# Kernel tuning notes

Measured on AMD Instinct MI355X. Metric: run time of the kernel, lower is better.

## Reference

```python
import jax, jax.numpy as jnp
import numpy as np

DIM = 768
HEADS = 12
SCALE = DIM ** (-0.5)  # NOTE: original scales by full dim, not per-head dim


def setup_inputs() -> dict:
    key = jax.random.key(0)
    k1, k2, k3 = jax.random.split(key, 3)
    b, n = 4, 2048
    x = jax.random.normal(k1, (b, n, DIM), dtype=jnp.float32)
    # torch Linear layout: weight [out_features, in_features]
    w_qkv = jax.random.normal(k2, (3 * DIM, DIM), dtype=jnp.float32) * (DIM ** -0.5)
    b_qkv = jnp.zeros((3 * DIM,), dtype=jnp.float32)
    w_out = jax.random.normal(k3, (DIM, DIM), dtype=jnp.float32) * (DIM ** -0.5)
    b_out = jnp.zeros((DIM,), dtype=jnp.float32)
    return {"x": x, "w_qkv": w_qkv, "b_qkv": b_qkv, "w_out": w_out, "b_out": b_out}


def reference(x, w_qkv, b_qkv, w_out, b_out):
    b, n, dim = x.shape
    h = HEADS
    d = dim // h
    qkv = x @ w_qkv.T + b_qkv                       # [b, n, 3*dim]
    # rearrange 'b n (qkv h d) -> qkv b h n d'
    qkv = qkv.reshape(b, n, 3, h, d).transpose(2, 0, 3, 1, 4)
    q, k, v = qkv[0], qkv[1], qkv[2]                # each [b, h, n, d]
    dots = jnp.einsum('bhid,bhjd->bhij', q, k) * SCALE
    attn = jax.nn.softmax(dots, axis=-1)
    out = jnp.einsum('bhij,bhjd->bhid', attn, v)    # [b, h, n, d]
    out = out.transpose(0, 2, 1, 3).reshape(b, n, h * d)
    out = out @ w_out.T + b_out
    return out
```

## Files before the change

### kernel.cpp

```cpp
#include <hip/hip_runtime.h>
#include <hip/hip_bf16.h>
#include <stdint.h>
#include <math.h>

#define HEADS 12
#define HD 64
#define NB 4
#define NSEQ 2048
#define DIM 768
#define MROWS (NB*NSEQ)
#define QKV_OUT (3*DIM)
#define SCALE 0.03608439182435161f
#define QSCALE (0.03608439182435161f * 1.4426950408889634f)
#define RESCALE_THR 8.0f

typedef __bf16 bf16;
typedef __attribute__((ext_vector_type(8))) __bf16 bf16x8;
typedef __attribute__((ext_vector_type(4))) __bf16 bf16x4;
typedef __attribute__((ext_vector_type(4))) float f32x4;
typedef __attribute__((ext_vector_type(16))) float f32x16;
typedef unsigned int uint;

typedef __attribute__((address_space(1))) void gvoid_t;
typedef __attribute__((address_space(3))) void lvoid_t;
#define GLOAD_LDS16(src, dst) \
  __builtin_amdgcn_global_load_lds((gvoid_t*)(src), (lvoid_t*)(dst), 16, 0, 0)

__device__ __forceinline__ float max3f(float a, float b, float c) {
  return fmaxf(fmaxf(a, b), c);
}
__device__ __forceinline__ float fast_exp2(float x) {
  float r; asm("v_exp_f32 %0, %1" : "=v"(r) : "v"(x)); return r;
}

__global__ void k_cvt3(const float* __restrict__ x, const float* __restrict__ wqkv,
                       const float* __restrict__ wout,
                       bf16* __restrict__ xb, bf16* __restrict__ wqkvb,
                       bf16* __restrict__ woutb) {
  const int n0 = MROWS * DIM / 4, n1 = QKV_OUT * DIM / 4, n2 = DIM * DIM / 4;
  int i = blockIdx.x * blockDim.x + threadIdx.x;
  const float* src; bf16* dst;
  if (i < n0)           { src = x;    dst = xb; }
  else if (i < n0 + n1) { src = wqkv; dst = wqkvb; i -= n0; }
  else if (i < n0 + n1 + n2) { src = wout; dst = woutb; i -= n0 + n1; }
  else return;
  const f32x4 v = ((const f32x4*)src)[i];
  bf16x4 o;
#pragma unroll
  for (int j = 0; j < 4; ++j) o[j] = (bf16)v[j];
  ((bf16x4*)dst)[i] = o;
}

template<int ROWBYTES>
__device__ __forceinline__ void stage_swz(const bf16* g, int grow0, int gstride,
                                          int gcol0, char* ldsbuf) {
  constexpr int CPR = ROWBYTES / 16;
  const int t = threadIdx.x;
  const int wid = t >> 6;
#pragma unroll
  for (int call = 0; call < 2; ++call) {
    const int o = call * 4096 + t * 16;
    const int r = o / ROWBYTES;
    const int c = (o % ROWBYTES) / 16;
    const int cs = c ^ (r & (CPR - 1));
    const bf16* src = g + (long)(grow0 + r) * gstride + gcol0 + cs * 8;
    char* dst = ldsbuf + call * 4096 + wid * 1024;
    GLOAD_LDS16(src, dst);
  }
}

template<int ROWBYTES>
__device__ __forceinline__ bf16x8 frag_ld(const char* buf, int row, int chunk) {
  constexpr int CPR = ROWBYTES / 16;
  const int cs = chunk ^ (row & (CPR - 1));
  return *(const bf16x8*)(buf + row * ROWBYTES + cs * 16);
}

__device__ __forceinline__ uint cvtpk_bf16(float a, float b) {
  uint r; asm("v_cvt_pk_bf16_f32 %0, %1, %2" : "=v"(r) : "v"(a), "v"(b)); return r;
}
__device__ __forceinline__ void plswap(uint &a, uint &b) {
  asm("v_permlane32_swap_b32 %0, %1" : "+v"(a), "+v"(b));
}
__device__ __forceinline__ void build_pfrags(const f32x16 &p, bf16x8 *f) {
  union { uint u[4]; bf16x8 v; } A, B;
  uint a0 = cvtpk_bf16(p[0], p[1]),  b0 = cvtpk_bf16(p[4], p[5]);   plswap(a0, b0);
  uint a1 = cvtpk_bf16(p[2], p[3]),  b1 = cvtpk_bf16(p[6], p[7]);   plswap(a1, b1);
  A.u[0] = a0; A.u[1] = a1; A.u[2] = b0; A.u[3] = b1;
  uint a2 = cvtpk_bf16(p[8], p[9]),  b2 = cvtpk_bf16(p[12], p[13]); plswap(a2, b2);
  uint a3 = cvtpk_bf16(p[10], p[11]), b3 = cvtpk_bf16(p[14], p[15]); plswap(a3, b3);
  B.u[0] = a2; B.u[1] = a3; B.u[2] = b2; B.u[3] = b3;
  f[0] = A.v; f[1] = B.v;
}

__device__ __forceinline__ void gemm_core(const bf16* __restrict__ A, const bf16* __restrict__ Bm,
                                          int m0, int n0, f32x4 acc[4][4], char* lds) {
  const int t = threadIdx.x;
  const int lane = t & 63, wid = t >> 6;
  const int lr = lane & 15, l4 = lane >> 4;
  const int wm = wid >> 1, wn = wid & 1;
#pragma unroll
  for (int i = 0; i < 4; ++i)
#pragma unroll
    for (int j = 0; j < 4; ++j) acc[i][j] = f32x4{0.f, 0.f, 0.f, 0.f};

  stage_swz<64>(A, m0, DIM, 0, lds);
  stage_swz<64>(Bm, n0, DIM, 0, lds + 16384);
  __syncthreads();
  int cur = 0;
  const int NT = DIM / 32;
  for (int kt = 0; kt < NT; ++kt) {
    char* Acur = lds + cur * 8192;
    char* Bcur = lds + 16384 + cur * 8192;
    if (kt + 1 < NT) {
      stage_swz<64>(A, m0, DIM, (kt + 1) * 32, lds + (cur ^ 1) * 8192);
      stage_swz<64>(Bm, n0, DIM, (kt + 1) * 32, lds + 16384 + (cur ^ 1) * 8192);
    }
    bf16x8 af[4], bfr[4];
#pragma unroll
    for (int i = 0; i < 4; ++i) af[i] = frag_ld<64>(Acur, wm * 64 + i * 16 + lr, l4);
#pragma unroll
    for (int j = 0; j < 4; ++j) bfr[j] = frag_ld<64>(Bcur, wn * 64 + j * 16 + lr, l4);
#pragma unroll
    for (int i = 0; i < 4; ++i)
#pragma unroll
      for (int j = 0; j < 4; ++j)
        acc[i][j] = __builtin_amdgcn_mfma_f32_16x16x32_bf16(af[i], bfr[j], acc[i][j], 0, 0, 0);
    __syncthreads();
    cur ^= 1;
  }
}

__global__ void __launch_bounds__(256) k_qkv_gemm(const bf16* __restrict__ xb,
                                                  const bf16* __restrict__ wb,
                                                  const float* __restrict__ bqkv,
                                                  bf16* __restrict__ qb,
                                                  bf16* __restrict__ kb,
                                                  bf16* __restrict__ vtb) {
  __shared__ alignas(128) char lds[32768];
  const int m0 = blockIdx.x * 128;
  const int n0 = blockIdx.y * 128;
  f32x4 acc[4][4];
  gemm_core(xb, wb, m0, n0, acc, lds);

  const int t = threadIdx.x;
  const int lane = t & 63, wid = t >> 6;
  const int lr = lane & 15, l4 = lane >> 4;
  const int wm = wid >> 1, wn = wid & 1;
#pragma unroll
  for (int j = 0; j < 4; ++j) {
    const int o = n0 + wn * 64 + j * 16 + lr;
    const float bias = bqkv[o];
    const int region = o / DIM;
    const int oc = o - region * DIM;
    const int h = oc >> 6, d = oc & 63;
#pragma unroll
    for (int i = 0; i < 4; ++i) {
      const int mb = m0 + wm * 64 + i * 16 + l4 * 4;
      const int bb = mb >> 11;
      const int nn = mb & 2047;
      if (region == 2) {
        bf16x4 pk;
#pragma unroll
        for (int r = 0; r < 4; ++r) pk[r] = (bf16)(acc[i][j][r] + bias);
        *(bf16x4*)(vtb + ((long)((bb * HEADS + h) * HD + d)) * NSEQ + nn) = pk;
      } else {
#pragma unroll
        for (int r = 0; r < 4; ++r) {
          const float v = acc[i][j][r] + bias;
          const long idx = ((long)((bb * HEADS + h) * NSEQ + (nn + r))) * HD + d;
          if (region == 0) qb[idx] = (bf16)(v * QSCALE);
          else             kb[idx] = (bf16)v;
        }
      }
    }
  }
}

__global__ void __launch_bounds__(256) k_attn(const bf16* __restrict__ qb,
                                              const bf16* __restrict__ kb,
                                              const bf16* __restrict__ vtb,
                                              bf16* __restrict__ ob) {
  __shared__ alignas(128) char lds[32768];
  const int bh = blockIdx.x;
  const int qt = blockIdx.y;
  const int t = threadIdx.x;
  const int lane = t & 63, wid = t >> 6;
  const int l31 = lane & 31, hi = lane >> 5;
  const bf16* qg = qb + (long)bh * NSEQ * HD;
  const bf16* kg = kb + (long)bh * NSEQ * HD;
  const bf16* vg = vtb + (long)bh * HD * NSEQ;
  const int q0w = qt * 128 + wid * 32;

  bf16x8 bq[4];
#pragma unroll
  for (int ks = 0; ks < 4; ++ks)
    bq[ks] = *(const bf16x8*)(qg + (long)(q0w + l31) * HD + ks * 16 + hi * 8);

  f32x16 ot0, ot1;
#pragma unroll
  for (int r = 0; r < 16; ++r) { ot0[r] = 0.f; ot1[r] = 0.f; }
  float m_run = -1.0e30f, l_run = 0.f;

  stage_swz<128>(kg, 0, HD, 0, lds);
  stage_swz<128>(vg, 0, NSEQ, 0, lds + 16384);
  __syncthreads();
  int cur = 0;
  for (int kt = 0; kt < NSEQ / 64; ++kt) {
    char* Kcur = lds + cur * 8192;
    char* Vcur = lds + 16384 + cur * 8192;
    if (kt + 1 < NSEQ / 64) {
      stage_swz<128>(kg, (kt + 1) * 64, HD, 0, lds + (cur ^ 1) * 8192);
      stage_swz<128>(vg, 0, NSEQ, (kt + 1) * 64, lds + 16384 + (cur ^ 1) * 8192);
    }
    f32x16 s0, s1;
#pragma unroll
    for (int r = 0; r < 16; ++r) { s0[r] = 0.f; s1[r] = 0.f; }
    __builtin_amdgcn_s_setprio(1);
#pragma unroll
    for (int ks = 0; ks < 4; ++ks) {
      const bf16x8 ak0 = frag_ld<128>(Kcur, l31, ks * 2 + hi);
      s0 = __builtin_amdgcn_mfma_f32_32x32x16_bf16(ak0, bq[ks], s0, 0, 0, 0);
      const bf16x8 ak1 = frag_ld<128>(Kcur, 32 + l31, ks * 2 + hi);
      s1 = __builtin_amdgcn_mfma_f32_32x32x16_bf16(ak1, bq[ks], s1, 0, 0, 0);
    }
    __builtin_amdgcn_s_setprio(0);
    float u0 = max3f(s0[0], s0[1], s0[2]);
    float u1 = max3f(s0[3], s0[4], s0[5]);
    float u2 = max3f(s0[6], s0[7], s0[8]);
    float u3 = max3f(s0[9], s0[10], s0[11]);
    float u4 = max3f(s0[12], s0[13], s0[14]);
    float u5 = max3f(s0[15], s1[0], s1[1]);
    float u6 = max3f(s1[2], s1[3], s1[4]);
    float u7 = max3f(s1[5], s1[6], s1[7]);
    float u8 = max3f(s1[8], s1[9], s1[10]);
    float u9 = max3f(s1[11], s1[12], s1[13]);
    float ua = fmaxf(s1[14], s1[15]);
    u0 = max3f(u0, u1, u2);
    u3 = max3f(u3, u4, u5);
    u6 = max3f(u6, u7, u8);
    u9 = max3f(u9, ua, u0);
    float mx = max3f(u3, u6, u9);
    mx = fmaxf(mx, __shfl_xor(mx, 32));
    if (__any(mx - m_run > RESCALE_THR)) {
      const float mn = fmaxf(m_run, mx);
      const float alpha = fast_exp2(m_run - mn);
      m_run = mn;
      l_run *= alpha;
#pragma unroll
      for (int r = 0; r < 16; ++r) { ot0[r] *= alpha; ot1[r] *= alpha; }
    }
    float rs0 = 0.f, rs1 = 0.f;
#pragma unroll
    for (int r = 0; r < 16; ++r) {
      s0[r] = fast_exp2(s0[r] - m_run); rs0 += s0[r];
      s1[r] = fast_exp2(s1[r] - m_run); rs1 += s1[r];
    }
    float rs = rs0 + rs1;
    rs += __shfl_xor(rs, 32);
    l_run += rs;
    bf16x8 pf[4];
    build_pfrags(s0, &pf[0]);
    build_pfrags(s1, &pf[2]);
    __builtin_amdgcn_s_setprio(1);
#pragma unroll
    for (int s = 0; s < 4; ++s) {
      const bf16x8 av0 = frag_ld<128>(Vcur, l31, s * 2 + hi);
      ot0 = __builtin_amdgcn_mfma_f32_32x32x16_bf16(av0, pf[s], ot0, 0, 0, 0);
      const bf16x8 av1 = frag_ld<128>(Vcur, 32 + l31, s * 2 + hi);
      ot1 = __builtin_amdgcn_mfma_f32_32x32x16_bf16(av1, pf[s], ot1, 0, 0, 0);
    }
    __builtin_amdgcn_s_setprio(0);
    __syncthreads();
    cur ^= 1;
  }
  const float inv = 1.f / l_run;
#pragma unroll
  for (int r = 0; r < 16; ++r) { ot0[r] *= inv; ot1[r] *= inv; }
  __syncthreads();
  char* tw = lds + wid * 4352;
#pragma unroll
  for (int g = 0; g < 4; ++g) {
    uint2 w0, w1;
    w0.x = cvtpk_bf16(ot0[4 * g], ot0[4 * g + 1]);
    w0.y = cvtpk_bf16(ot0[4 * g + 2], ot0[4 * g + 3]);
    w1.x = cvtpk_bf16(ot1[4 * g], ot1[4 * g + 1]);
    w1.y = cvtpk_bf16(ot1[4 * g + 2], ot1[4 * g + 3]);
    const int d0 = 8 * g + 4 * hi;
    *(uint2*)(tw + l31 * 136 + d0 * 2) = w0;
    *(uint2*)(tw + l31 * 136 + (32 + d0) * 2) = w1;
  }
  const int b_ = bh / HEADS, h_ = bh - b_ * HEADS;
#pragma unroll
  for (int pass = 0; pass < 4; ++pass) {
    const int row = pass * 8 + (lane >> 3);
    const bf16x8 vv = *(const bf16x8*)(tw + row * 136 + (lane & 7) * 16);
    *(bf16x8*)(ob + ((long)(b_ * NSEQ + q0w + row)) * DIM + h_ * 64 + (lane & 7) * 8) = vv;
  }
}

__global__ void __launch_bounds__(256) k_out_gemm(const bf16* __restrict__ ab,
                                                  const bf16* __restrict__ wob,
                                                  const float* __restrict__ bout,
                                                  float* __restrict__ out) {
  __shared__ alignas(128) char lds[32768];
  const int m0 = blockIdx.x * 128;
  const int n0 = blockIdx.y * 128;
  f32x4 acc[4][4];
  gemm_core(ab, wob, m0, n0, acc, lds);

  const int t = threadIdx.x;
  const int lane = t & 63, wid = t >> 6;
  const int lr = lane & 15, l4 = lane >> 4;
  const int wm = wid >> 1, wn = wid & 1;
#pragma unroll
  for (int j = 0; j < 4; ++j) {
    const int o = n0 + wn * 64 + j * 16 + lr;
    const float bias = bout[o];
#pragma unroll
    for (int i = 0; i < 4; ++i) {
      const int mb = m0 + wm * 64 + i * 16 + l4 * 4;
#pragma unroll
      for (int r = 0; r < 4; ++r)
        out[(long)(mb + r) * DIM + o] = acc[i][j][r] + bias;
    }
  }
}

extern "C" void kernel_launch(void* const* d_in, const int* in_sizes, int n_in,
                              void* d_out, int out_size, void* d_ws, size_t ws_size,
                              hipStream_t stream) {
  const float* x    = (const float*)d_in[0];
  const float* wqkv = (const float*)d_in[1];
  const float* bqkv = (const float*)d_in[2];
  const float* wout = (const float*)d_in[3];
  const float* bout = (const float*)d_in[4];
  float* out = (float*)d_out;
  char* ws = (char*)d_ws;

  bf16* xb    = (bf16*)(ws);
  bf16* wqkvb = (bf16*)(ws + 12582912);
  bf16* woutb = (bf16*)(ws + 16121856);
  bf16* qb    = (bf16*)(ws + 17301504);
  bf16* kb    = (bf16*)(ws + 29884416);
  bf16* vtb   = (bf16*)(ws + 42467328);
  bf16* ab    = (bf16*)(ws + 55050240);

  const int ncvt4 = MROWS * DIM / 4 + QKV_OUT * DIM / 4 + DIM * DIM / 4;
  k_cvt3<<<(ncvt4 + 255) / 256, 256, 0, stream>>>(x, wqkv, wout, xb, wqkvb, woutb);

  k_qkv_gemm<<<dim3(MROWS / 128, QKV_OUT / 128), 256, 0, stream>>>(xb, wqkvb, bqkv, qb, kb, vtb);
  k_attn<<<dim3(NB * HEADS, NSEQ / 128), 256, 0, stream>>>(qb, kb, vtb, ab);
  k_out_gemm<<<dim3(MROWS / 128, DIM / 128), 256, 0, stream>>>(ab, woutb, bout, out);
}
```

Measured before the change: 156.1 us.

## Swap GEMM operand order for vectorized epilogue stores and hoist attention staging addresses

```diff
diff --git a/kernel.cpp b/kernel.cpp
--- a/kernel.cpp
+++ b/kernel.cpp
@@ -10,7 +10,6 @@
 #define DIM 768
 #define MROWS (NB*NSEQ)
 #define QKV_OUT (3*DIM)
-#define SCALE 0.03608439182435161f
 #define QSCALE (0.03608439182435161f * 1.4426950408889634f)
 #define RESCALE_THR 8.0f
 
@@ -31,6 +30,12 @@
 }
 __device__ __forceinline__ float fast_exp2(float x) {
   float r; asm("v_exp_f32 %0, %1" : "=v"(r) : "v"(x)); return r;
+}
+__device__ __forceinline__ uint cvtpk_bf16(float a, float b) {
+  uint r; asm("v_cvt_pk_bf16_f32 %0, %1, %2" : "=v"(r) : "v"(a), "v"(b)); return r;
+}
+__device__ __forceinline__ void plswap(uint &a, uint &b) {
+  asm("v_permlane32_swap_b32 %0, %1" : "+v"(a), "+v"(b));
 }
 
 __global__ void k_cvt3(const float* __restrict__ x, const float* __restrict__ wqkv,
@@ -76,12 +81,6 @@
   return *(const bf16x8*)(buf + row * ROWBYTES + cs * 16);
 }
 
-__device__ __forceinline__ uint cvtpk_bf16(float a, float b) {
-  uint r; asm("v_cvt_pk_bf16_f32 %0, %1, %2" : "=v"(r) : "v"(a), "v"(b)); return r;
-}
-__device__ __forceinline__ void plswap(uint &a, uint &b) {
-  asm("v_permlane32_swap_b32 %0, %1" : "+v"(a), "+v"(b));
-}
 __device__ __forceinline__ void build_pfrags(const f32x16 &p, bf16x8 *f) {
   union { uint u[4]; bf16x8 v; } A, B;
   uint a0 = cvtpk_bf16(p[0], p[1]),  b0 = cvtpk_bf16(p[4], p[5]);   plswap(a0, b0);
@@ -140,38 +139,52 @@
   __shared__ alignas(128) char lds[32768];
   const int m0 = blockIdx.x * 128;
   const int n0 = blockIdx.y * 128;
-  f32x4 acc[4][4];
-  gemm_core(xb, wb, m0, n0, acc, lds);
-
+  const int region = n0 / DIM;
   const int t = threadIdx.x;
   const int lane = t & 63, wid = t >> 6;
   const int lr = lane & 15, l4 = lane >> 4;
   const int wm = wid >> 1, wn = wid & 1;
-#pragma unroll
-  for (int j = 0; j < 4; ++j) {
-    const int o = n0 + wn * 64 + j * 16 + lr;
-    const float bias = bqkv[o];
-    const int region = o / DIM;
-    const int oc = o - region * DIM;
-    const int h = oc >> 6, d = oc & 63;
-#pragma unroll
-    for (int i = 0; i < 4; ++i) {
-      const int mb = m0 + wm * 64 + i * 16 + l4 * 4;
-      const int bb = mb >> 11;
-      const int nn = mb & 2047;
-      if (region == 2) {
+  f32x4 acc[4][4];
+
+  if (region < 2) {
+    gemm_core(wb, xb, n0, m0, acc, lds);
+    bf16* dst0 = (region == 0) ? qb : kb;
+#pragma unroll
+    for (int j = 0; j < 4; ++j) {
+      const int mb = m0 + wn * 64 + j * 16 + lr;
+      const int bb = mb >> 11, nn = mb & 2047;
+#pragma unroll
+      for (int i = 0; i < 4; ++i) {
+        const int o = n0 + wm * 64 + i * 16 + l4 * 4;
+        const f32x4 b4 = *(const f32x4*)(bqkv + o);
+        const int oc = o - region * DIM;
+        const int h = oc >> 6, d = oc & 63;
+        bf16x4 pk;
+#pragma unroll
+        for (int r = 0; r < 4; ++r) {
+          float v = acc[i][j][r] + b4[r];
+          if (region == 0) v *= QSCALE;
+          pk[r] = (bf16)v;
+        }
+        *(bf16x4*)(dst0 + ((long)((bb * HEADS + h) * NSEQ + nn)) * HD + d) = pk;
+      }
+    }
+  } else {
+    gemm_core(xb, wb, m0, n0, acc, lds);
+#pragma unroll
+    for (int j = 0; j < 4; ++j) {
+      const int o = n0 + wn * 64 + j * 16 + lr;
+      const float bias = bqkv[o];
+      const int oc = o - 2 * DIM;
+      const int h = oc >> 6, d = oc & 63;
+#pragma unroll
+      for (int i = 0; i < 4; ++i) {
+        const int mb = m0 + wm * 64 + i * 16 + l4 * 4;
+        const int bb = mb >> 11, nn = mb & 2047;
         bf16x4 pk;
 #pragma unroll
         for (int r = 0; r < 4; ++r) pk[r] = (bf16)(acc[i][j][r] + bias);
         *(bf16x4*)(vtb + ((long)((bb * HEADS + h) * HD + d)) * NSEQ + nn) = pk;
-      } else {
-#pragma unroll
-        for (int r = 0; r < 4; ++r) {
-          const float v = acc[i][j][r] + bias;
-          const long idx = ((long)((bb * HEADS + h) * NSEQ + (nn + r))) * HD + d;
-          if (region == 0) qb[idx] = (bf16)(v * QSCALE);
-          else             kb[idx] = (bf16)v;
-        }
       }
     }
   }
@@ -182,6 +195,7 @@
                                               const bf16* __restrict__ vtb,
                                               bf16* __restrict__ ob) {
   __shared__ alignas(128) char lds[32768];
+  char* ldsc = lds;
   const int bh = blockIdx.x;
   const int qt = blockIdx.y;
   const int t = threadIdx.x;
@@ -197,31 +211,49 @@
   for (int ks = 0; ks < 4; ++ks)
     bq[ks] = *(const bf16x8*)(qg + (long)(q0w + l31) * HD + ks * 16 + hi * 8);
 
+  const int rbase = l31 * 128 + (((hi ^ l31) & 7) << 4);
+
+  const int o0 = t * 16, o1 = 4096 + t * 16;
+  const int r0 = o0 >> 7, cs0 = ((o0 & 127) >> 4) ^ (r0 & 7);
+  const int r1 = o1 >> 7, cs1 = ((o1 & 127) >> 4) ^ (r1 & 7);
+  const bf16* ksA = kg + r0 * 64 + cs0 * 8;
+  const bf16* ksB = kg + r1 * 64 + cs1 * 8;
+  const bf16* vsA = vg + (long)r0 * NSEQ + cs0 * 8;
+  const bf16* vsB = vg + (long)r1 * NSEQ + cs1 * 8;
+  const int dofs = wid << 10;
+
   f32x16 ot0, ot1;
 #pragma unroll
   for (int r = 0; r < 16; ++r) { ot0[r] = 0.f; ot1[r] = 0.f; }
   float m_run = -1.0e30f, l_run = 0.f;
 
-  stage_swz<128>(kg, 0, HD, 0, lds);
-  stage_swz<128>(vg, 0, NSEQ, 0, lds + 16384);
+  GLOAD_LDS16(ksA, ldsc + dofs);
+  GLOAD_LDS16(ksB, ldsc + 4096 + dofs);
+  GLOAD_LDS16(vsA, ldsc + 16384 + dofs);
+  GLOAD_LDS16(vsB, ldsc + 20480 + dofs);
   __syncthreads();
   int cur = 0;
   for (int kt = 0; kt < NSEQ / 64; ++kt) {
-    char* Kcur = lds + cur * 8192;
-    char* Vcur = lds + 16384 + cur * 8192;
     if (kt + 1 < NSEQ / 64) {
-      stage_swz<128>(kg, (kt + 1) * 64, HD, 0, lds + (cur ^ 1) * 8192);
-      stage_swz<128>(vg, 0, NSEQ, (kt + 1) * 64, lds + 16384 + (cur ^ 1) * 8192);
-    }
+      const int nb = (cur ^ 1) << 13;
+      const int ko = (kt + 1) * 4096;
+      const int vo = (kt + 1) * 64;
+      GLOAD_LDS16(ksA + ko, ldsc + nb + dofs);
+      GLOAD_LDS16(ksB + ko, ldsc + nb + 4096 + dofs);
+      GLOAD_LDS16(vsA + vo, ldsc + nb + 16384 + dofs);
+      GLOAD_LDS16(vsB + vo, ldsc + nb + 20480 + dofs);
+    }
+    const int tb = rbase + (cur << 13);
     f32x16 s0, s1;
 #pragma unroll
     for (int r = 0; r < 16; ++r) { s0[r] = 0.f; s1[r] = 0.f; }
     __builtin_amdgcn_s_setprio(1);
 #pragma unroll
     for (int ks = 0; ks < 4; ++ks) {
-      const bf16x8 ak0 = frag_ld<128>(Kcur, l31, ks * 2 + hi);
+      const int a = tb ^ (ks << 5);
+      const bf16x8 ak0 = *(const bf16x8*)(ldsc + a);
       s0 = __builtin_amdgcn_mfma_f32_32x32x16_bf16(ak0, bq[ks], s0, 0, 0, 0);
-      const bf16x8 ak1 = frag_ld<128>(Kcur, 32 + l31, ks * 2 + hi);
+      const bf16x8 ak1 = *(const bf16x8*)(ldsc + a + 4096);
       s1 = __builtin_amdgcn_mfma_f32_32x32x16_bf16(ak1, bq[ks], s1, 0, 0, 0);
     }
     __builtin_amdgcn_s_setprio(0);
@@ -256,24 +288,24 @@
       s0[r] = fast_exp2(s0[r] - m_run); rs0 += s0[r];
       s1[r] = fast_exp2(s1[r] - m_run); rs1 += s1[r];
     }
-    float rs = rs0 + rs1;
-    rs += __shfl_xor(rs, 32);
-    l_run += rs;
+    l_run += rs0 + rs1;
     bf16x8 pf[4];
     build_pfrags(s0, &pf[0]);
     build_pfrags(s1, &pf[2]);
     __builtin_amdgcn_s_setprio(1);
 #pragma unroll
     for (int s = 0; s < 4; ++s) {
-      const bf16x8 av0 = frag_ld<128>(Vcur, l31, s * 2 + hi);
+      const int a = tb ^ (s << 5);
+      const bf16x8 av0 = *(const bf16x8*)(ldsc + a + 16384);
       ot0 = __builtin_amdgcn_mfma_f32_32x32x16_bf16(av0, pf[s], ot0, 0, 0, 0);
-      const bf16x8 av1 = frag_ld<128>(Vcur, 32 + l31, s * 2 + hi);
+      const bf16x8 av1 = *(const bf16x8*)(ldsc + a + 20480);
       ot1 = __builtin_amdgcn_mfma_f32_32x32x16_bf16(av1, pf[s], ot1, 0, 0, 0);
     }
     __builtin_amdgcn_s_setprio(0);
     __syncthreads();
     cur ^= 1;
   }
+  l_run += __shfl_xor(l_run, 32);
   const float inv = 1.f / l_run;
 #pragma unroll
   for (int r = 0; r < 16; ++r) { ot0[r] *= inv; ot1[r] *= inv; }
@@ -307,7 +339,7 @@
   const int m0 = blockIdx.x * 128;
   const int n0 = blockIdx.y * 128;
   f32x4 acc[4][4];
-  gemm_core(ab, wob, m0, n0, acc, lds);
+  gemm_core(wob, ab, n0, m0, acc, lds);
 
   const int t = threadIdx.x;
   const int lane = t & 63, wid = t >> 6;
@@ -315,14 +347,12 @@
   const int wm = wid >> 1, wn = wid & 1;
 #pragma unroll
   for (int j = 0; j < 4; ++j) {
-    const int o = n0 + wn * 64 + j * 16 + lr;
-    const float bias = bout[o];
+    const int mb = m0 + wn * 64 + j * 16 + lr;
 #pragma unroll
     for (int i = 0; i < 4; ++i) {
-      const int mb = m0 + wm * 64 + i * 16 + l4 * 4;
-#pragma unroll
-      for (int r = 0; r < 4; ++r)
-        out[(long)(mb + r) * DIM + o] = acc[i][j][r] + bias;
+      const int o = n0 + wm * 64 + i * 16 + l4 * 4;
+      const f32x4 v = acc[i][j] + *(const f32x4*)(bout + o);
+      *(f32x4*)(out + (long)mb * DIM + o) = v;
     }
   }
 }
```

New measurement: 155.9 us. No clear change (-0.1%).
